# Kernel tuning notes

Hardware: AMD Instinct MI355X
Metric: run time of the kernel (lower is better)

The kernel has to match this reference:

```python
import jax, jax.numpy as jnp
import numpy as np

NEG_INF = -1e9


def setup_inputs() -> dict:
    key = jax.random.key(0)
    k1, k2, k3, k4, k5, k6 = jax.random.split(key, 6)
    B, P, N, C, H = 32, 512, 64, 9, 128
    polylines = jax.random.normal(k1, (B, P, N, C), dtype=jnp.float32)
    polylines_mask = jax.random.uniform(k2, (B, P, N)) > 0.1
    # MLP params (Linear(C,H) -> ReLU -> Linear(H,H)), torch-style init scale
    W1 = jax.random.uniform(k3, (C, H), minval=-1.0, maxval=1.0) / jnp.sqrt(C)
    b1 = jax.random.uniform(k4, (H,), minval=-1.0, maxval=1.0) / jnp.sqrt(C)
    W2 = jax.random.uniform(k5, (H, H), minval=-1.0, maxval=1.0) / jnp.sqrt(H)
    b2 = jax.random.uniform(k6, (H,), minval=-1.0, maxval=1.0) / jnp.sqrt(H)
    return {"polylines": polylines, "polylines_mask": polylines_mask,
            "W1": W1, "b1": b1, "W2": W2, "b2": b2}


def reference(polylines, polylines_mask, W1, b1, W2, b2):
    # Point MLP applied to all points (invalid ones are overwritten below,
    # identical math to the torch masked-gather version).
    h = jax.nn.relu(jnp.einsum('bpnc,ch->bpnh', polylines, W1) + b1)
    feat = jnp.einsum('bpnh,hd->bpnd', h, W2) + b2  # [B,P,N,H]
    feat = jnp.where(polylines_mask[..., None], feat, NEG_INF)
    pooled = jnp.max(feat, axis=2)  # [B,P,H]
    # Polylines with no valid points pooled to NEG_INF -> zero them out.
    any_valid = jnp.any(polylines_mask, axis=2)  # [B,P]
    return jnp.where(any_valid[..., None], pooled, 0.0)
```

## Files before the change

kernel.cpp:

```cpp
#include <hip/hip_runtime.h>


using bf16x8 = __attribute__((ext_vector_type(8))) short;
using f32x4  = __attribute__((ext_vector_type(4))) float;

#define MFMA32(A,B,C) __builtin_amdgcn_mfma_f32_16x16x32_bf16((A),(B),(C),0,0,0)

__device__ __forceinline__ f32x4 vmax4(f32x4 a, f32x4 b) {
  return __builtin_elementwise_max(a, b);
}

__device__ __forceinline__ unsigned short f2bf(float f) {
  union { float f; unsigned int u; } v; v.f = f;
  unsigned int r = v.u + 0x7fffu + ((v.u >> 16) & 1u);
  return (unsigned short)(r >> 16);
}

__device__ __forceinline__ unsigned int pk2(float a, float b) {
  unsigned int r;
  asm("v_cvt_pk_bf16_f32 %0, %1, %2" : "=v"(r) : "v"(a), "v"(b));
  return r;
}

__device__ __forceinline__ f32x4 shfl_xor4(f32x4 v, int m) {
  f32x4 r;
  r[0] = __shfl_xor(v[0], m);
  r[1] = __shfl_xor(v[1], m);
  r[2] = __shfl_xor(v[2], m);
  r[3] = __shfl_xor(v[3], m);
  return r;
}

__global__ void prep1(const float* __restrict__ W1, const float* __restrict__ W2,
                      const void* __restrict__ mask,
                      unsigned short* __restrict__ w1sw, unsigned short* __restrict__ w2sw,
                      int* __restrict__ flag) {
  int b = blockIdx.x, t = threadIdx.x;
  if (b == 0) {
    __shared__ int cnt;
    if (t == 0) cnt = 0;
    __syncthreads();
    const unsigned char* mb = (const unsigned char*)mask;
    int local = 0;
    for (int i = t * 16; i < t * 16 + 16; i++) local += (mb[i] != 0) ? 1 : 0;
    atomicAdd(&cnt, local);
    __syncthreads();
    if (t == 0) *flag = (cnt > 2800) ? 1 : 0;
  } else if (b <= 2) {
    int e = (b - 1) * 256 + t;
    int lane = e & 63, grp = e >> 6;
    int li = lane & 15, q = lane >> 4;
    int h = grp * 16 + li;
    int c0 = q * 8;
    #pragma unroll
    for (int j = 0; j < 8; j++) {
      int c = c0 + j;
      w1sw[e * 8 + j] = f2bf((c < 9) ? W1[c * 128 + h] : 0.f);
    }
  } else {
    int e = (b - 3) * 256 + t;
    if (e < 2048) {
      int lane = e & 63, grp = e >> 6;
      int wr = grp >> 4, sub = grp & 15;
      int ks = sub >> 2, td = sub & 3;
      int li = lane & 15, q = lane >> 4;
      int d = wr * 64 + td * 16 + li;
      int h0 = ks * 32 + q * 8;
      #pragma unroll
      for (int j = 0; j < 8; j++)
        w2sw[e * 8 + j] = f2bf(W2[(h0 + j) * 128 + d]);
    }
  }
}

__global__ __launch_bounds__(256, 4) void poly_main_k(
    const float* __restrict__ X, const void* __restrict__ mask,
    const float* __restrict__ b1g, const float* __restrict__ b2g,
    const unsigned short* __restrict__ w1sw, const unsigned short* __restrict__ w2sw,
    const int* __restrict__ flagp, float* __restrict__ out)
{
  __shared__ __align__(16) unsigned char smem[37376];
  unsigned short* Hb = (unsigned short*)smem;
  float*          Xs = (float*)(smem + 32768);

  const int tid  = threadIdx.x;
  const int lane = tid & 63;
  const int w    = tid >> 6;
  const int wr   = w >> 1, wc = w & 1;
  const int li   = lane & 15, q = lane >> 4;

  {
    const char* xg = (const char*)X + (long long)blockIdx.x * 4608;
    __builtin_amdgcn_global_load_lds(
        (const __attribute__((address_space(1))) unsigned int*)(xg + tid * 16),
        (__attribute__((address_space(3))) unsigned int*)((char*)Xs + w * 1024),
        16, 0, 0);
    if (tid < 32)
      __builtin_amdgcn_global_load_lds(
          (const __attribute__((address_space(1))) unsigned int*)(xg + 4096 + tid * 16),
          (__attribute__((address_space(3))) unsigned int*)((char*)Xs + 4096),
          16, 0, 0);
  }

  float mf[4];
  {
    int flag = *flagp;
    long long mb = (long long)blockIdx.x * 128 + wc * 64 + li;
    if (flag) {
      const unsigned char* mp = (const unsigned char*)mask;
      #pragma unroll
      for (int tm = 0; tm < 4; tm++) mf[tm] = mp[mb + tm * 16] ? 0.f : -4e9f;
    } else {
      const int* mp = (const int*)mask;
      #pragma unroll
      for (int tm = 0; tm < 4; tm++) mf[tm] = mp[mb + tm * 16] ? 0.f : -4e9f;
    }
  }

  __syncthreads();

  bf16x8 bx[4];
  #pragma unroll
  for (int tm = 0; tm < 4; tm++) {
    int m = wc * 64 + tm * 16 + li;
    const float* xr = Xs + m * 9;
    union { bf16x8 v; unsigned int u[4]; } uu;
    uu.u[0] = uu.u[1] = uu.u[2] = uu.u[3] = 0u;
    if (q == 0) {
      uu.u[0] = pk2(xr[0], xr[1]); uu.u[1] = pk2(xr[2], xr[3]);
      uu.u[2] = pk2(xr[4], xr[5]); uu.u[3] = pk2(xr[6], xr[7]);
    } else if (q == 1) {
      uu.u[0] = pk2(xr[8], 0.f);
    }
    bx[tm] = uu.v;
  }

  #pragma unroll
  for (int th = 0; th < 4; th++) {
    bf16x8 a1 = *(const bf16x8*)(w1sw + ((wr * 4 + th) * 64 + lane) * 8);
    f32x4 bv = *(const f32x4*)(b1g + wr * 64 + th * 16 + q * 4);
    f32x4 acc[4];
    #pragma unroll
    for (int tm = 0; tm < 4; tm++) acc[tm] = bv;
    #pragma unroll
    for (int tm = 0; tm < 4; tm++) acc[tm] = MFMA32(a1, bx[tm], acc[tm]);
    #pragma unroll
    for (int tm = 0; tm < 4; tm++) {
      int m = wc * 64 + tm * 16 + li;
      f32x4 v = vmax4(acc[tm], f32x4{0.f, 0.f, 0.f, 0.f});
      uint2 hv;
      hv.x = pk2(v[0], v[1]);
      hv.y = pk2(v[2], v[3]);
      int chunk = (wr * 8 + th * 2 + (q >> 1)) ^ li;
      *(uint2*)(Hb + m * 128 + chunk * 8 + (q & 1) * 4) = hv;
    }
  }
  __syncthreads();

  f32x4 pooled[4];
  #pragma unroll
  for (int tm = 0; tm < 4; tm++) {
    int m = wc * 64 + tm * 16 + li;
    f32x4 acc[4];
    #pragma unroll
    for (int td = 0; td < 4; td++) acc[td] = f32x4{0.f, 0.f, 0.f, 0.f};
    #pragma unroll
    for (int ks = 0; ks < 4; ks++) {
      int chunk = (ks * 4 + q) ^ li;
      bf16x8 bb = *(const bf16x8*)(Hb + m * 128 + chunk * 8);
      #pragma unroll
      for (int td = 0; td < 4; td++) {
        bf16x8 a2 = *(const bf16x8*)(w2sw + (((wr * 16 + ks * 4 + td) * 64) + lane) * 8);
        acc[td] = MFMA32(a2, bb, acc[td]);
      }
    }
    if (tm == 0) {
      #pragma unroll
      for (int td = 0; td < 4; td++) pooled[td] = acc[td] + mf[0];
    } else {
      #pragma unroll
      for (int td = 0; td < 4; td++) pooled[td] = vmax4(pooled[td], acc[td] + mf[tm]);
    }
  }

  #pragma unroll
  for (int td = 0; td < 4; td++) {
    #pragma unroll
    for (int sm = 1; sm < 16; sm <<= 1)
      pooled[td] = vmax4(pooled[td], shfl_xor4(pooled[td], sm));
  }

  if (li == 0) {
    float* op = out + (long long)blockIdx.x * 256 + wc * 128 + wr * 64 + q * 4;
    #pragma unroll
    for (int td = 0; td < 4; td++) {
      f32x4 v = pooled[td] + *(const f32x4*)(b2g + wr * 64 + td * 16 + q * 4);
      #pragma unroll
      for (int j = 0; j < 4; j++) if (v[j] < -1e8f) v[j] = 0.f;
      *(f32x4*)(op + td * 16) = v;
    }
  }
}

extern "C" void kernel_launch(void* const* d_in, const int* in_sizes, int n_in,
                              void* d_out, int out_size, void* d_ws, size_t ws_size,
                              hipStream_t stream) {
  const float* X    = (const float*)d_in[0];
  const void*  mask = d_in[1];
  const float* W1   = (const float*)d_in[2];
  const float* b1   = (const float*)d_in[3];
  const float* W2   = (const float*)d_in[4];
  const float* b2   = (const float*)d_in[5];
  float* out = (float*)d_out;

  unsigned short* w1sw = (unsigned short*)d_ws;
  unsigned short* w2sw = (unsigned short*)((char*)d_ws + 8192);
  int* flag            = (int*)((char*)d_ws + 40960);

  prep1<<<11, 256, 0, stream>>>(W1, W2, mask, w1sw, w2sw, flag);
  poly_main_k<<<8192, 256, 0, stream>>>(X, mask, b1, b2, w1sw, w2sw, flag, out);
}
```

Before: 145.5 us.

## Keep hidden activations in registers via permlane swaps, one polyline per wave

Each wave now processes one whole polyline (all 128 hidden and output features) instead of splitting work across a 2x2 wave grid. The first-layer MFMA outputs are rearranged into the second-layer B-operand layout with v_permlane32/16 swaps, so the LDS round trip for the hidden activations and both block barriers are gone. LDS use shrinks to the input staging only, which can raise occupancy. In exchange each wave holds more accumulators and weight fragments, so register pressure rises, and the grid is halved.

```diff
diff --git a/kernel.cpp b/kernel.cpp
--- a/kernel.cpp
+++ b/kernel.cpp
@@ -79,33 +79,33 @@
     const unsigned short* __restrict__ w1sw, const unsigned short* __restrict__ w2sw,
     const int* __restrict__ flagp, float* __restrict__ out)
 {
-  __shared__ __align__(16) unsigned char smem[37376];
-  unsigned short* Hb = (unsigned short*)smem;
-  float*          Xs = (float*)(smem + 32768);
+  __shared__ __align__(16) unsigned char smem[9216];
 
   const int tid  = threadIdx.x;
   const int lane = tid & 63;
   const int w    = tid >> 6;
-  const int wr   = w >> 1, wc = w & 1;
   const int li   = lane & 15, q = lane >> 4;
+  const long long poly = (long long)blockIdx.x * 4 + w;
 
   {
-    const char* xg = (const char*)X + (long long)blockIdx.x * 4608;
+    const char* xg = (const char*)X + poly * 2304;
+    char* xl = (char*)smem + w * 2304;
     __builtin_amdgcn_global_load_lds(
-        (const __attribute__((address_space(1))) unsigned int*)(xg + tid * 16),
-        (__attribute__((address_space(3))) unsigned int*)((char*)Xs + w * 1024),
-        16, 0, 0);
-    if (tid < 32)
+        (const __attribute__((address_space(1))) unsigned int*)(xg + lane * 16),
+        (__attribute__((address_space(3))) unsigned int*)xl, 16, 0, 0);
+    __builtin_amdgcn_global_load_lds(
+        (const __attribute__((address_space(1))) unsigned int*)(xg + 1024 + lane * 16),
+        (__attribute__((address_space(3))) unsigned int*)(xl + 1024), 16, 0, 0);
+    if (lane < 16)
       __builtin_amdgcn_global_load_lds(
-          (const __attribute__((address_space(1))) unsigned int*)(xg + 4096 + tid * 16),
-          (__attribute__((address_space(3))) unsigned int*)((char*)Xs + 4096),
-          16, 0, 0);
+          (const __attribute__((address_space(1))) unsigned int*)(xg + 2048 + lane * 16),
+          (__attribute__((address_space(3))) unsigned int*)(xl + 2048), 16, 0, 0);
   }
 
   float mf[4];
   {
     int flag = *flagp;
-    long long mb = (long long)blockIdx.x * 128 + wc * 64 + li;
+    long long mb = poly * 64 + li;
     if (flag) {
       const unsigned char* mp = (const unsigned char*)mask;
       #pragma unroll
@@ -117,84 +117,95 @@
     }
   }
 
-  __syncthreads();
-
-  bf16x8 bx[4];
+  asm volatile("s_waitcnt vmcnt(0)" ::: "memory");
+
+  const float* Xw = (const float*)(smem + w * 2304);
+
+  f32x4 pooled[8];
   #pragma unroll
-  for (int tm = 0; tm < 4; tm++) {
-    int m = wc * 64 + tm * 16 + li;
-    const float* xr = Xs + m * 9;
-    union { bf16x8 v; unsigned int u[4]; } uu;
-    uu.u[0] = uu.u[1] = uu.u[2] = uu.u[3] = 0u;
-    if (q == 0) {
-      uu.u[0] = pk2(xr[0], xr[1]); uu.u[1] = pk2(xr[2], xr[3]);
-      uu.u[2] = pk2(xr[4], xr[5]); uu.u[3] = pk2(xr[6], xr[7]);
-    } else if (q == 1) {
-      uu.u[0] = pk2(xr[8], 0.f);
-    }
-    bx[tm] = uu.v;
+  for (int hf = 0; hf < 2; hf++) {
+    bf16x8 bx2[2];
+    #pragma unroll
+    for (int t = 0; t < 2; t++) {
+      const float* xr = Xw + ((hf * 2 + t) * 16 + li) * 9;
+      union { bf16x8 v; unsigned int u[4]; } uu;
+      uu.u[0] = uu.u[1] = uu.u[2] = uu.u[3] = 0u;
+      if (q == 0) {
+        uu.u[0] = pk2(xr[0], xr[1]); uu.u[1] = pk2(xr[2], xr[3]);
+        uu.u[2] = pk2(xr[4], xr[5]); uu.u[3] = pk2(xr[6], xr[7]);
+      } else if (q == 1) {
+        uu.u[0] = pk2(xr[8], 0.f);
+      }
+      bx2[t] = uu.v;
+    }
+
+    unsigned int Pp[8][2][2];
+    #pragma unroll
+    for (int th = 0; th < 8; th++) {
+      bf16x8 a1 = *(const bf16x8*)(w1sw + (th * 64 + lane) * 8);
+      f32x4 bv = *(const f32x4*)(b1g + th * 16 + q * 4);
+      f32x4 acc[2];
+      acc[0] = bv; acc[1] = bv;
+      acc[0] = MFMA32(a1, bx2[0], acc[0]);
+      acc[1] = MFMA32(a1, bx2[1], acc[1]);
+      #pragma unroll
+      for (int t = 0; t < 2; t++) {
+        f32x4 v = vmax4(acc[t], f32x4{0.f, 0.f, 0.f, 0.f});
+        Pp[th][t][0] = pk2(v[0], v[1]);
+        Pp[th][t][1] = pk2(v[2], v[3]);
+      }
+    }
+
+    #pragma unroll
+    for (int t = 0; t < 2; t++) {
+      const int tm = hf * 2 + t;
+      f32x4 acc2[8];
+      #pragma unroll
+      for (int td = 0; td < 8; td++) acc2[td] = f32x4{0.f, 0.f, 0.f, 0.f};
+      #pragma unroll
+      for (int ks = 0; ks < 4; ks++) {
+        #pragma unroll
+        for (int p = 0; p < 2; p++) {
+          asm volatile("v_permlane32_swap_b32 %0, %1"
+                       : "+v"(Pp[2 * ks][t][p]), "+v"(Pp[2 * ks + 1][t][p]));
+          asm volatile("v_permlane16_swap_b32 %0, %1"
+                       : "+v"(Pp[2 * ks][t][p]), "+v"(Pp[2 * ks + 1][t][p]));
+        }
+        union { bf16x8 v; unsigned int u[4]; } bh;
+        bh.u[0] = Pp[2 * ks][t][0];
+        bh.u[1] = Pp[2 * ks][t][1];
+        bh.u[2] = Pp[2 * ks + 1][t][0];
+        bh.u[3] = Pp[2 * ks + 1][t][1];
+        #pragma unroll
+        for (int td = 0; td < 8; td++) {
+          bf16x8 a2 = *(const bf16x8*)(
+              w2sw + ((((td >> 2) * 16 + ks * 4 + (td & 3)) * 64) + lane) * 8);
+          acc2[td] = MFMA32(a2, bh.v, acc2[td]);
+        }
+      }
+      if (tm == 0) {
+        #pragma unroll
+        for (int td = 0; td < 8; td++) pooled[td] = acc2[td] + mf[0];
+      } else {
+        #pragma unroll
+        for (int td = 0; td < 8; td++)
+          pooled[td] = vmax4(pooled[td], acc2[td] + mf[tm]);
+      }
+    }
   }
 
   #pragma unroll
-  for (int th = 0; th < 4; th++) {
-    bf16x8 a1 = *(const bf16x8*)(w1sw + ((wr * 4 + th) * 64 + lane) * 8);
-    f32x4 bv = *(const f32x4*)(b1g + wr * 64 + th * 16 + q * 4);
-    f32x4 acc[4];
-    #pragma unroll
-    for (int tm = 0; tm < 4; tm++) acc[tm] = bv;
-    #pragma unroll
-    for (int tm = 0; tm < 4; tm++) acc[tm] = MFMA32(a1, bx[tm], acc[tm]);
-    #pragma unroll
-    for (int tm = 0; tm < 4; tm++) {
-      int m = wc * 64 + tm * 16 + li;
-      f32x4 v = vmax4(acc[tm], f32x4{0.f, 0.f, 0.f, 0.f});
-      uint2 hv;
-      hv.x = pk2(v[0], v[1]);
-      hv.y = pk2(v[2], v[3]);
-      int chunk = (wr * 8 + th * 2 + (q >> 1)) ^ li;
-      *(uint2*)(Hb + m * 128 + chunk * 8 + (q & 1) * 4) = hv;
-    }
-  }
-  __syncthreads();
-
-  f32x4 pooled[4];
-  #pragma unroll
-  for (int tm = 0; tm < 4; tm++) {
-    int m = wc * 64 + tm * 16 + li;
-    f32x4 acc[4];
-    #pragma unroll
-    for (int td = 0; td < 4; td++) acc[td] = f32x4{0.f, 0.f, 0.f, 0.f};
-    #pragma unroll
-    for (int ks = 0; ks < 4; ks++) {
-      int chunk = (ks * 4 + q) ^ li;
-      bf16x8 bb = *(const bf16x8*)(Hb + m * 128 + chunk * 8);
-      #pragma unroll
-      for (int td = 0; td < 4; td++) {
-        bf16x8 a2 = *(const bf16x8*)(w2sw + (((wr * 16 + ks * 4 + td) * 64) + lane) * 8);
-        acc[td] = MFMA32(a2, bb, acc[td]);
-      }
-    }
-    if (tm == 0) {
-      #pragma unroll
-      for (int td = 0; td < 4; td++) pooled[td] = acc[td] + mf[0];
-    } else {
-      #pragma unroll
-      for (int td = 0; td < 4; td++) pooled[td] = vmax4(pooled[td], acc[td] + mf[tm]);
-    }
-  }
-
-  #pragma unroll
-  for (int td = 0; td < 4; td++) {
+  for (int td = 0; td < 8; td++) {
     #pragma unroll
     for (int sm = 1; sm < 16; sm <<= 1)
       pooled[td] = vmax4(pooled[td], shfl_xor4(pooled[td], sm));
   }
 
   if (li == 0) {
-    float* op = out + (long long)blockIdx.x * 256 + wc * 128 + wr * 64 + q * 4;
-    #pragma unroll
-    for (int td = 0; td < 4; td++) {
-      f32x4 v = pooled[td] + *(const f32x4*)(b2g + wr * 64 + td * 16 + q * 4);
+    float* op = out + poly * 128 + q * 4;
+    #pragma unroll
+    for (int td = 0; td < 8; td++) {
+      f32x4 v = pooled[td] + *(const f32x4*)(b2g + td * 16 + q * 4);
       #pragma unroll
       for (int j = 0; j < 4; j++) if (v[j] < -1e8f) v[j] = 0.f;
       *(f32x4*)(op + td * 16) = v;
@@ -218,5 +229,5 @@
   int* flag            = (int*)((char*)d_ws + 40960);
 
   prep1<<<11, 256, 0, stream>>>(W1, W2, mask, w1sw, w2sw, flag);
-  poly_main_k<<<8192, 256, 0, stream>>>(X, mask, b1, b2, w1sw, w2sw, flag, out);
-}
+  poly_main_k<<<4096, 256, 0, stream>>>(X, mask, b1, b2, w1sw, w2sw, flag, out);
+}
```

Measured after the change: 270.0 us. 1.86x slower.

## Keep hidden activations in registers via permlane swaps and fold b1 into W1

Applied to the files above, without the earlier changes.

The kernel is restructured so each wave handles two whole polylines for one half of the output features. The first-layer MFMA output is reshuffled in registers with permlane32/16 swaps to form the second-layer B operand, which removes the LDS round-trip for the hidden activations and both block barriers. The b1 bias is folded into W1 as an extra input channel set to 1.0. W1 and W2 fragments are loaded once into registers and reused across polylines. In exchange, register pressure rises (launch bounds drop to 3 waves) and the grid is halved, and the first layer's work is duplicated across the two d-halves.

```diff
diff --git a/kernel.cpp b/kernel.cpp
--- a/kernel.cpp
+++ b/kernel.cpp
@@ -31,8 +31,8 @@
   return r;
 }
 
-__global__ void prep1(const float* __restrict__ W1, const float* __restrict__ W2,
-                      const void* __restrict__ mask,
+__global__ void prep1(const float* __restrict__ W1, const float* __restrict__ b1,
+                      const float* __restrict__ W2, const void* __restrict__ mask,
                       unsigned short* __restrict__ w1sw, unsigned short* __restrict__ w2sw,
                       int* __restrict__ flag) {
   int b = blockIdx.x, t = threadIdx.x;
@@ -55,7 +55,8 @@
     #pragma unroll
     for (int j = 0; j < 8; j++) {
       int c = c0 + j;
-      w1sw[e * 8 + j] = f2bf((c < 9) ? W1[c * 128 + h] : 0.f);
+      float v = (c < 9) ? W1[c * 128 + h] : ((c == 9) ? b1[h] : 0.f);
+      w1sw[e * 8 + j] = f2bf(v);
     }
   } else {
     int e = (b - 3) * 256 + t;
@@ -73,131 +74,146 @@
   }
 }
 
-__global__ __launch_bounds__(256, 4) void poly_main_k(
+__global__ __launch_bounds__(256, 3) void poly_main_k(
     const float* __restrict__ X, const void* __restrict__ mask,
-    const float* __restrict__ b1g, const float* __restrict__ b2g,
+    const float* __restrict__ b2g,
     const unsigned short* __restrict__ w1sw, const unsigned short* __restrict__ w2sw,
     const int* __restrict__ flagp, float* __restrict__ out)
 {
-  __shared__ __align__(16) unsigned char smem[37376];
-  unsigned short* Hb = (unsigned short*)smem;
-  float*          Xs = (float*)(smem + 32768);
+  __shared__ __align__(16) unsigned char smem[18432];
 
   const int tid  = threadIdx.x;
   const int lane = tid & 63;
   const int w    = tid >> 6;
-  const int wr   = w >> 1, wc = w & 1;
   const int li   = lane & 15, q = lane >> 4;
+  const int pair = w >> 1, dhalf = w & 1;
+  const long long poly0 = (long long)blockIdx.x * 4 + pair * 2;
 
   {
-    const char* xg = (const char*)X + (long long)blockIdx.x * 4608;
-    __builtin_amdgcn_global_load_lds(
-        (const __attribute__((address_space(1))) unsigned int*)(xg + tid * 16),
-        (__attribute__((address_space(3))) unsigned int*)((char*)Xs + w * 1024),
-        16, 0, 0);
-    if (tid < 32)
+    const char* xg = (const char*)X + poly0 * 2304;
+    char* xl = (char*)smem + w * 4608;
+    #pragma unroll
+    for (int k = 0; k < 4; k++)
       __builtin_amdgcn_global_load_lds(
-          (const __attribute__((address_space(1))) unsigned int*)(xg + 4096 + tid * 16),
-          (__attribute__((address_space(3))) unsigned int*)((char*)Xs + 4096),
-          16, 0, 0);
+          (const __attribute__((address_space(1))) unsigned int*)(xg + k * 1024 + lane * 16),
+          (__attribute__((address_space(3))) unsigned int*)(xl + k * 1024), 16, 0, 0);
+    if (lane < 32)
+      __builtin_amdgcn_global_load_lds(
+          (const __attribute__((address_space(1))) unsigned int*)(xg + 4096 + lane * 16),
+          (__attribute__((address_space(3))) unsigned int*)(xl + 4096), 16, 0, 0);
   }
 
-  float mf[4];
-  {
-    int flag = *flagp;
-    long long mb = (long long)blockIdx.x * 128 + wc * 64 + li;
-    if (flag) {
-      const unsigned char* mp = (const unsigned char*)mask;
-      #pragma unroll
-      for (int tm = 0; tm < 4; tm++) mf[tm] = mp[mb + tm * 16] ? 0.f : -4e9f;
-    } else {
-      const int* mp = (const int*)mask;
-      #pragma unroll
-      for (int tm = 0; tm < 4; tm++) mf[tm] = mp[mb + tm * 16] ? 0.f : -4e9f;
-    }
-  }
-
-  __syncthreads();
-
-  bf16x8 bx[4];
+  const int flag = *flagp;
+
+  bf16x8 w1f[8];
   #pragma unroll
-  for (int tm = 0; tm < 4; tm++) {
-    int m = wc * 64 + tm * 16 + li;
-    const float* xr = Xs + m * 9;
-    union { bf16x8 v; unsigned int u[4]; } uu;
-    uu.u[0] = uu.u[1] = uu.u[2] = uu.u[3] = 0u;
-    if (q == 0) {
-      uu.u[0] = pk2(xr[0], xr[1]); uu.u[1] = pk2(xr[2], xr[3]);
-      uu.u[2] = pk2(xr[4], xr[5]); uu.u[3] = pk2(xr[6], xr[7]);
-    } else if (q == 1) {
-      uu.u[0] = pk2(xr[8], 0.f);
-    }
-    bx[tm] = uu.v;
-  }
-
+  for (int th = 0; th < 8; th++)
+    w1f[th] = *(const bf16x8*)(w1sw + (th * 64 + lane) * 8);
+
+  bf16x8 w2f[4][4];
   #pragma unroll
-  for (int th = 0; th < 4; th++) {
-    bf16x8 a1 = *(const bf16x8*)(w1sw + ((wr * 4 + th) * 64 + lane) * 8);
-    f32x4 bv = *(const f32x4*)(b1g + wr * 64 + th * 16 + q * 4);
-    f32x4 acc[4];
-    #pragma unroll
-    for (int tm = 0; tm < 4; tm++) acc[tm] = bv;
-    #pragma unroll
-    for (int tm = 0; tm < 4; tm++) acc[tm] = MFMA32(a1, bx[tm], acc[tm]);
-    #pragma unroll
-    for (int tm = 0; tm < 4; tm++) {
-      int m = wc * 64 + tm * 16 + li;
-      f32x4 v = vmax4(acc[tm], f32x4{0.f, 0.f, 0.f, 0.f});
-      uint2 hv;
-      hv.x = pk2(v[0], v[1]);
-      hv.y = pk2(v[2], v[3]);
-      int chunk = (wr * 8 + th * 2 + (q >> 1)) ^ li;
-      *(uint2*)(Hb + m * 128 + chunk * 8 + (q & 1) * 4) = hv;
-    }
-  }
-  __syncthreads();
-
-  f32x4 pooled[4];
+  for (int ks = 0; ks < 4; ks++)
+    #pragma unroll
+    for (int td = 0; td < 4; td++)
+      w2f[ks][td] = *(const bf16x8*)(w2sw + ((dhalf * 16 + ks * 4 + td) * 64 + lane) * 8);
+
+  asm volatile("s_waitcnt vmcnt(0)" ::: "memory");
+
+  const float* Xw = (const float*)(smem + w * 4608);
+
   #pragma unroll
-  for (int tm = 0; tm < 4; tm++) {
-    int m = wc * 64 + tm * 16 + li;
-    f32x4 acc[4];
-    #pragma unroll
-    for (int td = 0; td < 4; td++) acc[td] = f32x4{0.f, 0.f, 0.f, 0.f};
-    #pragma unroll
-    for (int ks = 0; ks < 4; ks++) {
-      int chunk = (ks * 4 + q) ^ li;
-      bf16x8 bb = *(const bf16x8*)(Hb + m * 128 + chunk * 8);
+  for (int pl = 0; pl < 2; pl++) {
+    const long long poly = poly0 + pl;
+
+    float mf[4];
+    {
+      long long mb = poly * 64 + li;
+      if (flag) {
+        const unsigned char* mp = (const unsigned char*)mask;
+        #pragma unroll
+        for (int tm = 0; tm < 4; tm++) mf[tm] = mp[mb + tm * 16] ? 0.f : -4e9f;
+      } else {
+        const int* mp = (const int*)mask;
+        #pragma unroll
+        for (int tm = 0; tm < 4; tm++) mf[tm] = mp[mb + tm * 16] ? 0.f : -4e9f;
+      }
+    }
+
+    f32x4 pooled[4];
+    #pragma unroll
+    for (int mt = 0; mt < 4; mt++) {
+      const float* xr = Xw + pl * 576 + (mt * 16 + li) * 9;
+      union { bf16x8 v; unsigned int u[4]; } uu;
+      uu.u[0] = uu.u[1] = uu.u[2] = uu.u[3] = 0u;
+      if (q == 0) {
+        uu.u[0] = pk2(xr[0], xr[1]); uu.u[1] = pk2(xr[2], xr[3]);
+        uu.u[2] = pk2(xr[4], xr[5]); uu.u[3] = pk2(xr[6], xr[7]);
+      } else if (q == 1) {
+        uu.u[0] = pk2(xr[8], 1.0f);
+      }
+      const bf16x8 bx = uu.v;
+
+      unsigned int Pp[8][2];
+      #pragma unroll
+      for (int th = 0; th < 8; th++) {
+        f32x4 a = f32x4{0.f, 0.f, 0.f, 0.f};
+        a = MFMA32(w1f[th], bx, a);
+        f32x4 v = vmax4(a, f32x4{0.f, 0.f, 0.f, 0.f});
+        Pp[th][0] = pk2(v[0], v[1]);
+        Pp[th][1] = pk2(v[2], v[3]);
+      }
+
+      #pragma unroll
+      for (int ks = 0; ks < 4; ks++)
+        #pragma unroll
+        for (int p = 0; p < 2; p++) {
+          asm volatile("v_permlane32_swap_b32 %0, %1"
+                       : "+v"(Pp[2 * ks][p]), "+v"(Pp[2 * ks + 1][p]));
+          asm volatile("v_permlane16_swap_b32 %0, %1"
+                       : "+v"(Pp[2 * ks][p]), "+v"(Pp[2 * ks + 1][p]));
+        }
+
+      f32x4 acc2[4];
+      #pragma unroll
+      for (int td = 0; td < 4; td++) acc2[td] = f32x4{0.f, 0.f, 0.f, 0.f};
+      #pragma unroll
+      for (int ks = 0; ks < 4; ks++) {
+        union { bf16x8 v; unsigned int u[4]; } bh;
+        bh.u[0] = Pp[2 * ks][0];
+        bh.u[1] = Pp[2 * ks][1];
+        bh.u[2] = Pp[2 * ks + 1][0];
+        bh.u[3] = Pp[2 * ks + 1][1];
+        #pragma unroll
+        for (int td = 0; td < 4; td++)
+          acc2[td] = MFMA32(w2f[ks][td], bh.v, acc2[td]);
+      }
+
+      if (mt == 0) {
+        #pragma unroll
+        for (int td = 0; td < 4; td++) pooled[td] = acc2[td] + mf[0];
+      } else {
+        #pragma unroll
+        for (int td = 0; td < 4; td++)
+          pooled[td] = vmax4(pooled[td], acc2[td] + mf[mt]);
+      }
+    }
+
+    #pragma unroll
+    for (int td = 0; td < 4; td++) {
+      #pragma unroll
+      for (int sm = 1; sm < 16; sm <<= 1)
+        pooled[td] = vmax4(pooled[td], shfl_xor4(pooled[td], sm));
+    }
+
+    if (li == 0) {
+      float* op = out + poly * 128 + dhalf * 64 + q * 4;
       #pragma unroll
       for (int td = 0; td < 4; td++) {
-        bf16x8 a2 = *(const bf16x8*)(w2sw + (((wr * 16 + ks * 4 + td) * 64) + lane) * 8);
-        acc[td] = MFMA32(a2, bb, acc[td]);
-      }
-    }
-    if (tm == 0) {
-      #pragma unroll
-      for (int td = 0; td < 4; td++) pooled[td] = acc[td] + mf[0];
-    } else {
-      #pragma unroll
-      for (int td = 0; td < 4; td++) pooled[td] = vmax4(pooled[td], acc[td] + mf[tm]);
-    }
-  }
-
-  #pragma unroll
-  for (int td = 0; td < 4; td++) {
-    #pragma unroll
-    for (int sm = 1; sm < 16; sm <<= 1)
-      pooled[td] = vmax4(pooled[td], shfl_xor4(pooled[td], sm));
-  }
-
-  if (li == 0) {
-    float* op = out + (long long)blockIdx.x * 256 + wc * 128 + wr * 64 + q * 4;
-    #pragma unroll
-    for (int td = 0; td < 4; td++) {
-      f32x4 v = pooled[td] + *(const f32x4*)(b2g + wr * 64 + td * 16 + q * 4);
-      #pragma unroll
-      for (int j = 0; j < 4; j++) if (v[j] < -1e8f) v[j] = 0.f;
-      *(f32x4*)(op + td * 16) = v;
+        f32x4 v = pooled[td] + *(const f32x4*)(b2g + dhalf * 64 + td * 16 + q * 4);
+        #pragma unroll
+        for (int j = 0; j < 4; j++) if (v[j] < -1e8f) v[j] = 0.f;
+        *(f32x4*)(op + td * 16) = v;
+      }
     }
   }
 }
@@ -217,6 +233,6 @@
   unsigned short* w2sw = (unsigned short*)((char*)d_ws + 8192);
   int* flag            = (int*)((char*)d_ws + 40960);
 
-  prep1<<<11, 256, 0, stream>>>(W1, W2, mask, w1sw, w2sw, flag);
-  poly_main_k<<<8192, 256, 0, stream>>>(X, mask, b1, b2, w1sw, w2sw, flag, out);
-}
+  prep1<<<11, 256, 0, stream>>>(W1, b1, W2, mask, w1sw, w2sw, flag);
+  poly_main_k<<<4096, 256, 0, stream>>>(X, mask, b2, w1sw, w2sw, flag, out);
+}
```

Result: slower. 176.0 us (+21.0%).
